# Kernel tuning notes

Hardware: AMD Instinct MI355X
Metric: run time of the kernel (lower is better)

## Reference

```python
import jax, jax.numpy as jnp
import numpy as np
import math

D_MODEL = 1024
N_HEADS = 16
D_HEAD = D_MODEL // N_HEADS


def setup_inputs() -> dict:
    key = jax.random.key(0)
    ks = jax.random.split(key, 5)
    B, T, C = 4, 2048, D_MODEL
    s = 1.0 / math.sqrt(C)
    return {
        "x": jax.random.normal(ks[0], (B, T, C), dtype=jnp.float32),
        "qkv_w": jax.random.normal(ks[1], (3 * C, C), dtype=jnp.float32) * s,
        "qkv_b": jnp.zeros((3 * C,), dtype=jnp.float32),
        "out_w": jax.random.normal(ks[2], (C, C), dtype=jnp.float32) * s,
        "out_b": jnp.zeros((C,), dtype=jnp.float32),
    }


def reference(x, qkv_w, qkv_b, out_w, out_b):
    B, T, C = x.shape
    H, Dh = N_HEADS, D_HEAD
    qkv = x @ qkv_w.T + qkv_b              # [B,T,3C] (torch Linear: x W^T + b)
    q, k, v = jnp.split(qkv, 3, axis=-1)
    # [B,T,C] -> [B,H,T,Dh]
    q = q.reshape(B, T, H, Dh).transpose(0, 2, 1, 3)
    k = k.reshape(B, T, H, Dh).transpose(0, 2, 1, 3)
    v = v.reshape(B, T, H, Dh).transpose(0, 2, 1, 3)
    att = jnp.einsum("bhqd,bhkd->bhqk", q, k) / math.sqrt(Dh)
    causal = jnp.tril(jnp.ones((T, T), dtype=bool))  # True = keep
    att = jnp.where(causal, att, -jnp.inf)
    att = jax.nn.softmax(att, axis=-1)
    y = jnp.einsum("bhqk,bhkd->bhqd", att, v)
    y = y.transpose(0, 2, 1, 3).reshape(B, T, C)
    return y @ out_w.T + out_b
```

## Files before the change

### kernel.cpp

```cpp
#include <hip/hip_runtime.h>

typedef __attribute__((ext_vector_type(4))) float f32x4;
typedef __attribute__((ext_vector_type(16))) float f32x16;
typedef __attribute__((ext_vector_type(8))) __bf16 bf16x8;
typedef __attribute__((ext_vector_type(4))) __bf16 bf16x4;
typedef __attribute__((ext_vector_type(2))) unsigned u32x2;

#define MFMA_B16(a,b,c) __builtin_amdgcn_mfma_f32_16x16x32_bf16((a),(b),(c),0,0,0)
#define MFMA32(a,b,c)  __builtin_amdgcn_mfma_f32_32x32x16_bf16((a),(b),(c),0,0,0)

static constexpr int T_LEN  = 2048;
static constexpr int C_DIM  = 1024;
static constexpr int H_NUM  = 16;
static constexpr int D_HEADc = 64;
static constexpr float Q_PRESCALE = 0.125f * 1.4426950408889634f;

__device__ __forceinline__ void async16(const void* g, void* l) {
  __builtin_amdgcn_global_load_lds(
      (const __attribute__((address_space(1))) unsigned int*)g,
      (__attribute__((address_space(3))) unsigned int*)l, 16, 0, 0);
}

__device__ __forceinline__ unsigned cvtpk(float lo, float hi) {
  unsigned r;
  asm("v_cvt_pk_bf16_f32 %0, %1, %2" : "=v"(r) : "v"(lo), "v"(hi));
  return r;
}

__global__ __launch_bounds__(256) void cvt_kernel(const float* __restrict__ s,
                                                  __bf16* __restrict__ d, int n4) {
  int i = blockIdx.x * 256 + threadIdx.x;
  if (i >= n4) return;
  float4 f = reinterpret_cast<const float4*>(s)[i];
  bf16x4 o;
  o.x = (__bf16)f.x; o.y = (__bf16)f.y; o.z = (__bf16)f.z; o.w = (__bf16)f.w;
  reinterpret_cast<bf16x4*>(d)[i] = o;
}

__global__ __launch_bounds__(256) void gemm_qkv(const __bf16* __restrict__ A,
                                                const __bf16* __restrict__ W,
                                                const float* __restrict__ bias,
                                                __bf16* __restrict__ qb,
                                                __bf16* __restrict__ kb,
                                                __bf16* __restrict__ vb) {
  constexpr int K = 1024;
  __shared__ __bf16 As[128 * 64];
  __shared__ __bf16 Bs[128 * 64];
  const int tid = threadIdx.x;
  const int wid = tid >> 6, lane = tid & 63, l16 = lane & 15, lg = lane >> 4;
  const int r8 = lane >> 3, sl = lane & 7;
  const int r7 = l16 & 7;
  const int wm = wid >> 1, wn = wid & 1;
  const int m0 = blockIdx.x * 128, n0 = blockIdx.y * 128;

  f32x4 acc[4][4];
#pragma unroll
  for (int i = 0; i < 4; ++i)
#pragma unroll
    for (int j = 0; j < 4; ++j) acc[i][j] = f32x4{0.f, 0.f, 0.f, 0.f};

  for (int k0 = 0; k0 < K; k0 += 64) {
    __builtin_amdgcn_s_barrier();
#pragma unroll
    for (int it = 0; it < 4; ++it) {
      int chunk = it * 4 + wid;
      int row = chunk * 8 + r8;
      int scol = ((sl ^ (row & 7)) << 3);
      async16(A + (long)(m0 + row) * K + k0 + scol, &As[chunk * 512]);
      async16(W + (long)(n0 + row) * K + k0 + scol, &Bs[chunk * 512]);
    }
    asm volatile("s_waitcnt vmcnt(0)" ::: "memory");
    __builtin_amdgcn_s_barrier();
#pragma unroll
    for (int kt = 0; kt < 2; ++kt) {
      const int sw = ((((kt << 2) | lg) ^ r7) << 3);
      bf16x8 af[4], bfv[4];
#pragma unroll
      for (int mi = 0; mi < 4; ++mi)
        af[mi] = *reinterpret_cast<const bf16x8*>(&As[(wm * 64 + mi * 16 + l16) * 64 + sw]);
#pragma unroll
      for (int nt = 0; nt < 4; ++nt)
        bfv[nt] = *reinterpret_cast<const bf16x8*>(&Bs[(wn * 64 + nt * 16 + l16) * 64 + sw]);
#pragma unroll
      for (int mi = 0; mi < 4; ++mi)
#pragma unroll
        for (int nt = 0; nt < 4; ++nt)
          acc[mi][nt] = MFMA_B16(af[mi], bfv[nt], acc[mi][nt]);
    }
  }
#pragma unroll
  for (int mi = 0; mi < 4; ++mi)
#pragma unroll
    for (int nt = 0; nt < 4; ++nt)
#pragma unroll
      for (int r = 0; r < 4; ++r) {
        int m = m0 + wm * 64 + mi * 16 + lg * 4 + r;
        int n = n0 + wn * 64 + nt * 16 + l16;
        float val = acc[mi][nt][r] + bias[n];
        int which = n >> 10;
        int cc = n & 1023;
        int h = cc >> 6, d = cc & 63;
        long b = m >> 11;
        long t = m & 2047;
        if (which == 0) {
          qb[(((b * H_NUM + h) * T_LEN) + t) * D_HEADc + d] = (__bf16)(val * Q_PRESCALE);
        } else if (which == 1) {
          kb[(((b * H_NUM + h) * T_LEN) + t) * D_HEADc + d] = (__bf16)val;
        } else {
          vb[(((b * H_NUM + h) * D_HEADc) + d) * T_LEN + t] = (__bf16)val;
        }
      }
}

__global__ __launch_bounds__(256) void attn_kernel(const __bf16* __restrict__ q,
                                                   const __bf16* __restrict__ k,
                                                   const __bf16* __restrict__ vt,
                                                   __bf16* __restrict__ y) {
  __shared__ __bf16 Ks[2][64 * 64];
  __shared__ __bf16 Vs[2][64 * 64];
  const int tid = threadIdx.x;
  const int wid = tid >> 6, lane = tid & 63;
  const int l31 = lane & 31, hi = lane >> 5;
  const int r8 = lane >> 3, sl = lane & 7;
  const int r7 = l31 & 7;
  const int bid = blockIdx.x;
  const int qt = 15 - (bid >> 6);
  const int bh = bid & 63;
  const int q0 = qt * 128;
  const int qw = q0 + wid * 32;
  const int qglob = qw + l31;
  const __bf16* qg = q + (long)bh * T_LEN * D_HEADc;
  const __bf16* kg = k + (long)bh * T_LEN * D_HEADc;
  const __bf16* vg = vt + (long)bh * T_LEN * D_HEADc;

  bf16x8 qf[4];
#pragma unroll
  for (int dt = 0; dt < 4; ++dt)
    qf[dt] = *reinterpret_cast<const bf16x8*>(
        qg + (long)qglob * D_HEADc + dt * 16 + hi * 8);

  f32x16 o[2];
#pragma unroll
  for (int di = 0; di < 2; ++di)
#pragma unroll
    for (int r = 0; r < 16; ++r) o[di][r] = 0.f;
  float m = -3e38f, l = 0.f;

  auto stage = [&](int buf, int t) {
    const int k0s = t * 64;
#pragma unroll
    for (int it = 0; it < 2; ++it) {
      int chunk = it * 4 + wid;
      int row = chunk * 8 + r8;
      int scol = ((sl ^ (row & 7)) << 3);
      async16(kg + (long)(k0s + row) * D_HEADc + scol, &Ks[buf][chunk * 512]);
      async16(vg + (long)row * T_LEN + k0s + scol, &Vs[buf][chunk * 512]);
    }
  };

  const int ntiles = qt * 2 + 2;
  stage(0, 0);
  int cur = 0;
  for (int t = 0; t < ntiles; ++t) {
    if (t + 1 < ntiles) {
      stage(cur ^ 1, t + 1);
      asm volatile("s_waitcnt vmcnt(4)" ::: "memory");
    } else {
      asm volatile("s_waitcnt vmcnt(0)" ::: "memory");
    }
    __builtin_amdgcn_s_barrier();
    const int k0 = t * 64;
    if (k0 < qw + 32) {
      f32x16 s[2];
#pragma unroll
      for (int ki = 0; ki < 2; ++ki)
#pragma unroll
        for (int r = 0; r < 16; ++r) s[ki][r] = 0.f;
      __builtin_amdgcn_s_setprio(1);
#pragma unroll
      for (int dt = 0; dt < 4; ++dt) {
        const int swz = (((dt << 1) | hi) ^ r7) << 3;
        bf16x8 kf0 = *reinterpret_cast<const bf16x8*>(&Ks[cur][l31 * 64 + swz]);
        bf16x8 kf1 = *reinterpret_cast<const bf16x8*>(&Ks[cur][(32 + l31) * 64 + swz]);
        s[0] = MFMA32(kf0, qf[dt], s[0]);
        s[1] = MFMA32(kf1, qf[dt], s[1]);
      }
      __builtin_amdgcn_s_setprio(0);

      if (k0 + 63 > qw) {
#pragma unroll
        for (int r = 0; r < 16; ++r) {
          const int kb = (r & 3) + 8 * (r >> 2) + 4 * hi;
          if (k0 + kb > qglob) s[0][r] = -3e38f;
          if (k0 + 32 + kb > qglob) s[1][r] = -3e38f;
        }
      }
      float mx = -3e38f;
#pragma unroll
      for (int r = 0; r < 16; ++r) mx = fmaxf(mx, fmaxf(s[0][r], s[1][r]));
      mx = fmaxf(mx, __shfl_xor(mx, 32));
      if (!__all(mx <= m + 8.f)) {
        const float mn = fmaxf(m, mx);
        const float al = exp2f(m - mn);
        m = mn;
        l *= al;
#pragma unroll
        for (int di = 0; di < 2; ++di)
#pragma unroll
          for (int r = 0; r < 16; ++r) o[di][r] *= al;
      }
      float ls = 0.f;
      unsigned pb[4][4];
#pragma unroll
      for (int ki = 0; ki < 2; ++ki) {
#pragma unroll
        for (int r = 0; r < 16; ++r) {
          float e = exp2f(s[ki][r] - m);
          ls += e;
          s[ki][r] = e;
        }
        unsigned d0 = cvtpk(s[ki][0], s[ki][1]),   d1 = cvtpk(s[ki][2], s[ki][3]);
        unsigned d2 = cvtpk(s[ki][4], s[ki][5]),   d3 = cvtpk(s[ki][6], s[ki][7]);
        unsigned d4 = cvtpk(s[ki][8], s[ki][9]),   d5 = cvtpk(s[ki][10], s[ki][11]);
        unsigned d6 = cvtpk(s[ki][12], s[ki][13]), d7 = cvtpk(s[ki][14], s[ki][15]);
        u32x2 a = __builtin_amdgcn_permlane32_swap(d0, d2, false, false);
        u32x2 b = __builtin_amdgcn_permlane32_swap(d1, d3, false, false);
        pb[ki * 2][0] = a[0]; pb[ki * 2][1] = b[0];
        pb[ki * 2][2] = a[1]; pb[ki * 2][3] = b[1];
        u32x2 c = __builtin_amdgcn_permlane32_swap(d4, d6, false, false);
        u32x2 d = __builtin_amdgcn_permlane32_swap(d5, d7, false, false);
        pb[ki * 2 + 1][0] = c[0]; pb[ki * 2 + 1][1] = d[0];
        pb[ki * 2 + 1][2] = c[1]; pb[ki * 2 + 1][3] = d[1];
      }
      ls += __shfl_xor(ls, 32);
      l += ls;

      __builtin_amdgcn_s_setprio(1);
#pragma unroll
      for (int kt = 0; kt < 4; ++kt) {
        union { unsigned u[4]; bf16x8 v; } pu;
        pu.u[0] = pb[kt][0]; pu.u[1] = pb[kt][1];
        pu.u[2] = pb[kt][2]; pu.u[3] = pb[kt][3];
        const int swz = (((kt << 1) | hi) ^ r7) << 3;
        bf16x8 vf0 = *reinterpret_cast<const bf16x8*>(&Vs[cur][l31 * 64 + swz]);
        bf16x8 vf1 = *reinterpret_cast<const bf16x8*>(&Vs[cur][(32 + l31) * 64 + swz]);
        o[0] = MFMA32(vf0, pu.v, o[0]);
        o[1] = MFMA32(vf1, pu.v, o[1]);
      }
      __builtin_amdgcn_s_setprio(0);
    }
    __builtin_amdgcn_s_barrier();
    cur ^= 1;
  }

  const long bb = bh >> 4;
  const int h = bh & 15;
  const float inv = 1.f / l;
  const long row = bb * T_LEN + qglob;
#pragma unroll
  for (int di = 0; di < 2; ++di)
#pragma unroll
    for (int rr = 0; rr < 4; ++rr) {
      bf16x4 pk;
#pragma unroll
      for (int c = 0; c < 4; ++c) pk[c] = (__bf16)(o[di][rr * 4 + c] * inv);
      *reinterpret_cast<bf16x4*>(
          &y[row * C_DIM + h * D_HEADc + di * 32 + rr * 8 + hi * 4]) = pk;
    }
}

__global__ __launch_bounds__(256) void gemm_proj(const __bf16* __restrict__ A,
                                                 const __bf16* __restrict__ W,
                                                 const float* __restrict__ bias,
                                                 float* __restrict__ out) {
  constexpr int K = 1024;
  __shared__ __bf16 As[128 * 64];
  __shared__ __bf16 Bs[128 * 64];
  const int tid = threadIdx.x;
  const int wid = tid >> 6, lane = tid & 63, l16 = lane & 15, lg = lane >> 4;
  const int r8 = lane >> 3, sl = lane & 7;
  const int r7 = l16 & 7;
  const int wm = wid >> 1, wn = wid & 1;
  const int m0 = blockIdx.x * 128, n0 = blockIdx.y * 128;

  f32x4 acc[4][4];
#pragma unroll
  for (int i = 0; i < 4; ++i)
#pragma unroll
    for (int j = 0; j < 4; ++j) acc[i][j] = f32x4{0.f, 0.f, 0.f, 0.f};

  for (int k0 = 0; k0 < K; k0 += 64) {
    __builtin_amdgcn_s_barrier();
#pragma unroll
    for (int it = 0; it < 4; ++it) {
      int chunk = it * 4 + wid;
      int row = chunk * 8 + r8;
      int scol = ((sl ^ (row & 7)) << 3);
      async16(A + (long)(m0 + row) * K + k0 + scol, &As[chunk * 512]);
      async16(W + (long)(n0 + row) * K + k0 + scol, &Bs[chunk * 512]);
    }
    asm volatile("s_waitcnt vmcnt(0)" ::: "memory");
    __builtin_amdgcn_s_barrier();
#pragma unroll
    for (int kt = 0; kt < 2; ++kt) {
      const int sw = ((((kt << 2) | lg) ^ r7) << 3);
      bf16x8 af[4], bfv[4];
#pragma unroll
      for (int mi = 0; mi < 4; ++mi)
        af[mi] = *reinterpret_cast<const bf16x8*>(&As[(wm * 64 + mi * 16 + l16) * 64 + sw]);
#pragma unroll
      for (int nt = 0; nt < 4; ++nt)
        bfv[nt] = *reinterpret_cast<const bf16x8*>(&Bs[(wn * 64 + nt * 16 + l16) * 64 + sw]);
#pragma unroll
      for (int mi = 0; mi < 4; ++mi)
#pragma unroll
        for (int nt = 0; nt < 4; ++nt)
          acc[mi][nt] = MFMA_B16(af[mi], bfv[nt], acc[mi][nt]);
    }
  }
#pragma unroll
  for (int mi = 0; mi < 4; ++mi)
#pragma unroll
    for (int nt = 0; nt < 4; ++nt)
#pragma unroll
      for (int r = 0; r < 4; ++r) {
        long m = m0 + wm * 64 + mi * 16 + lg * 4 + r;
        int n = n0 + wn * 64 + nt * 16 + l16;
        out[m * C_DIM + n] = acc[mi][nt][r] + bias[n];
      }
}

extern "C" void kernel_launch(void* const* d_in, const int* in_sizes, int n_in,
                              void* d_out, int out_size, void* d_ws, size_t ws_size,
                              hipStream_t stream) {
  const float* x     = (const float*)d_in[0];
  const float* qkv_w = (const float*)d_in[1];
  const float* qkv_b = (const float*)d_in[2];
  const float* out_w = (const float*)d_in[3];
  const float* out_b = (const float*)d_in[4];
  float* out = (float*)d_out;

  const long NX  = 8192L * 1024;
  const long NWQ = 3072L * 1024;
  const long NWO = 1024L * 1024;
  const size_t need = (size_t)(5 * NX + NWQ + NWO) * 2;
  if (ws_size < need) return;

  __bf16* xb   = (__bf16*)d_ws;
  __bf16* wqkv = xb + NX;
  __bf16* wout = wqkv + NWQ;
  __bf16* qb   = wout + NWO;
  __bf16* kb   = qb + NX;
  __bf16* vb   = kb + NX;
  __bf16* yb   = vb + NX;

  cvt_kernel<<<(int)(NX / 4 / 256), 256, 0, stream>>>(x, xb, (int)(NX / 4));
  cvt_kernel<<<(int)(NWQ / 4 / 256), 256, 0, stream>>>(qkv_w, wqkv, (int)(NWQ / 4));
  cvt_kernel<<<(int)(NWO / 4 / 256), 256, 0, stream>>>(out_w, wout, (int)(NWO / 4));

  gemm_qkv<<<dim3(64, 24), 256, 0, stream>>>(xb, wqkv, qkv_b, qb, kb, vb);
  attn_kernel<<<dim3(1024), 256, 0, stream>>>(qb, kb, vb, yb);
  gemm_proj<<<dim3(64, 8), 256, 0, stream>>>(yb, wout, out_b, out);
}
```

Baseline: 196.4 us.

## Pair causal query tiles per block, fuse casts, and compute row sums via MFMA

The attention kernel now launches half as many blocks, and each block handles two query tiles (qt and 15-qt) in sequence so every block does the same causal work. The row-sum of softmax probabilities moves from scalar adds plus a shuffle to an extra MFMA against a vector of ones, and the row-max becomes a tree reduction. The three float-to-bf16 conversion launches become one kernel. In exchange there are fewer resident blocks, so latency hiding may drop, and each tile pair runs serially with a pipeline restart between phases.

```diff
diff --git a/kernel.cpp b/kernel.cpp
--- a/kernel.cpp
+++ b/kernel.cpp
@@ -27,14 +27,21 @@
   return r;
 }
 
-__global__ __launch_bounds__(256) void cvt_kernel(const float* __restrict__ s,
-                                                  __bf16* __restrict__ d, int n4) {
+__global__ __launch_bounds__(256) void cvt3_kernel(const float* __restrict__ a, __bf16* __restrict__ da, int na,
+                                                   const float* __restrict__ b, __bf16* __restrict__ db, int nb,
+                                                   const float* __restrict__ c, __bf16* __restrict__ dc, int nc) {
   int i = blockIdx.x * 256 + threadIdx.x;
-  if (i >= n4) return;
-  float4 f = reinterpret_cast<const float4*>(s)[i];
+  const float* s;
+  __bf16* d;
+  long j;
+  if (i < na) { s = a; d = da; j = i; }
+  else if (i < na + nb) { s = b; d = db; j = i - na; }
+  else if (i < na + nb + nc) { s = c; d = dc; j = i - na - nb; }
+  else return;
+  float4 f = reinterpret_cast<const float4*>(s)[j];
   bf16x4 o;
   o.x = (__bf16)f.x; o.y = (__bf16)f.y; o.z = (__bf16)f.z; o.w = (__bf16)f.w;
-  reinterpret_cast<bf16x4*>(d)[i] = o;
+  reinterpret_cast<bf16x4*>(d)[j] = o;
 }
 
 __global__ __launch_bounds__(256) void gemm_qkv(const __bf16* __restrict__ A,
@@ -124,27 +131,22 @@
   const int r8 = lane >> 3, sl = lane & 7;
   const int r7 = l31 & 7;
   const int bid = blockIdx.x;
-  const int qt = 15 - (bid >> 6);
+  const int pair = bid >> 6;
   const int bh = bid & 63;
-  const int q0 = qt * 128;
-  const int qw = q0 + wid * 32;
-  const int qglob = qw + l31;
   const __bf16* qg = q + (long)bh * T_LEN * D_HEADc;
   const __bf16* kg = k + (long)bh * T_LEN * D_HEADc;
   const __bf16* vg = vt + (long)bh * T_LEN * D_HEADc;
-
-  bf16x8 qf[4];
-#pragma unroll
-  for (int dt = 0; dt < 4; ++dt)
-    qf[dt] = *reinterpret_cast<const bf16x8*>(
-        qg + (long)qglob * D_HEADc + dt * 16 + hi * 8);
-
-  f32x16 o[2];
-#pragma unroll
-  for (int di = 0; di < 2; ++di)
-#pragma unroll
-    for (int r = 0; r < 16; ++r) o[di][r] = 0.f;
-  float m = -3e38f, l = 0.f;
+  const long bb = bh >> 4;
+  const int h = bh & 15;
+
+  union { unsigned short us[8]; bf16x8 v; } ones_u;
+#pragma unroll
+  for (int i = 0; i < 8; ++i) ones_u.us[i] = 0x3F80;
+  const bf16x8 ones = ones_u.v;
+
+  f32x16 z16;
+#pragma unroll
+  for (int r = 0; r < 16; ++r) z16[r] = 0.f;
 
   auto stage = [&](int buf, int t) {
     const int k0s = t * 64;
@@ -158,115 +160,141 @@
     }
   };
 
-  const int ntiles = qt * 2 + 2;
-  stage(0, 0);
-  int cur = 0;
-  for (int t = 0; t < ntiles; ++t) {
-    if (t + 1 < ntiles) {
-      stage(cur ^ 1, t + 1);
-      asm volatile("s_waitcnt vmcnt(4)" ::: "memory");
-    } else {
-      asm volatile("s_waitcnt vmcnt(0)" ::: "memory");
-    }
-    __builtin_amdgcn_s_barrier();
-    const int k0 = t * 64;
-    if (k0 < qw + 32) {
-      f32x16 s[2];
-#pragma unroll
-      for (int ki = 0; ki < 2; ++ki)
-#pragma unroll
-        for (int r = 0; r < 16; ++r) s[ki][r] = 0.f;
-      __builtin_amdgcn_s_setprio(1);
-#pragma unroll
-      for (int dt = 0; dt < 4; ++dt) {
-        const int swz = (((dt << 1) | hi) ^ r7) << 3;
-        bf16x8 kf0 = *reinterpret_cast<const bf16x8*>(&Ks[cur][l31 * 64 + swz]);
-        bf16x8 kf1 = *reinterpret_cast<const bf16x8*>(&Ks[cur][(32 + l31) * 64 + swz]);
-        s[0] = MFMA32(kf0, qf[dt], s[0]);
-        s[1] = MFMA32(kf1, qf[dt], s[1]);
-      }
-      __builtin_amdgcn_s_setprio(0);
-
-      if (k0 + 63 > qw) {
-#pragma unroll
-        for (int r = 0; r < 16; ++r) {
-          const int kb = (r & 3) + 8 * (r >> 2) + 4 * hi;
-          if (k0 + kb > qglob) s[0][r] = -3e38f;
-          if (k0 + 32 + kb > qglob) s[1][r] = -3e38f;
-        }
-      }
-      float mx = -3e38f;
-#pragma unroll
-      for (int r = 0; r < 16; ++r) mx = fmaxf(mx, fmaxf(s[0][r], s[1][r]));
-      mx = fmaxf(mx, __shfl_xor(mx, 32));
-      if (!__all(mx <= m + 8.f)) {
-        const float mn = fmaxf(m, mx);
-        const float al = exp2f(m - mn);
-        m = mn;
-        l *= al;
-#pragma unroll
-        for (int di = 0; di < 2; ++di)
-#pragma unroll
-          for (int r = 0; r < 16; ++r) o[di][r] *= al;
-      }
-      float ls = 0.f;
-      unsigned pb[4][4];
-#pragma unroll
-      for (int ki = 0; ki < 2; ++ki) {
-#pragma unroll
-        for (int r = 0; r < 16; ++r) {
-          float e = exp2f(s[ki][r] - m);
-          ls += e;
-          s[ki][r] = e;
-        }
-        unsigned d0 = cvtpk(s[ki][0], s[ki][1]),   d1 = cvtpk(s[ki][2], s[ki][3]);
-        unsigned d2 = cvtpk(s[ki][4], s[ki][5]),   d3 = cvtpk(s[ki][6], s[ki][7]);
-        unsigned d4 = cvtpk(s[ki][8], s[ki][9]),   d5 = cvtpk(s[ki][10], s[ki][11]);
-        unsigned d6 = cvtpk(s[ki][12], s[ki][13]), d7 = cvtpk(s[ki][14], s[ki][15]);
-        u32x2 a = __builtin_amdgcn_permlane32_swap(d0, d2, false, false);
-        u32x2 b = __builtin_amdgcn_permlane32_swap(d1, d3, false, false);
-        pb[ki * 2][0] = a[0]; pb[ki * 2][1] = b[0];
-        pb[ki * 2][2] = a[1]; pb[ki * 2][3] = b[1];
-        u32x2 c = __builtin_amdgcn_permlane32_swap(d4, d6, false, false);
-        u32x2 d = __builtin_amdgcn_permlane32_swap(d5, d7, false, false);
-        pb[ki * 2 + 1][0] = c[0]; pb[ki * 2 + 1][1] = d[0];
-        pb[ki * 2 + 1][2] = c[1]; pb[ki * 2 + 1][3] = d[1];
-      }
-      ls += __shfl_xor(ls, 32);
-      l += ls;
-
-      __builtin_amdgcn_s_setprio(1);
-#pragma unroll
-      for (int kt = 0; kt < 4; ++kt) {
-        union { unsigned u[4]; bf16x8 v; } pu;
-        pu.u[0] = pb[kt][0]; pu.u[1] = pb[kt][1];
-        pu.u[2] = pb[kt][2]; pu.u[3] = pb[kt][3];
-        const int swz = (((kt << 1) | hi) ^ r7) << 3;
-        bf16x8 vf0 = *reinterpret_cast<const bf16x8*>(&Vs[cur][l31 * 64 + swz]);
-        bf16x8 vf1 = *reinterpret_cast<const bf16x8*>(&Vs[cur][(32 + l31) * 64 + swz]);
-        o[0] = MFMA32(vf0, pu.v, o[0]);
-        o[1] = MFMA32(vf1, pu.v, o[1]);
-      }
-      __builtin_amdgcn_s_setprio(0);
-    }
-    __builtin_amdgcn_s_barrier();
-    cur ^= 1;
+  auto m3 = [](float a, float b, float c) { return fmaxf(fmaxf(a, b), c); };
+
+  for (int ph = 0; ph < 2; ++ph) {
+    const int qt = ph ? (15 - pair) : pair;
+    const int q0 = qt * 128;
+    const int qw = q0 + wid * 32;
+    const int qglob = qw + l31;
+
+    bf16x8 qf[4];
+#pragma unroll
+    for (int dt = 0; dt < 4; ++dt)
+      qf[dt] = *reinterpret_cast<const bf16x8*>(qg + (long)qglob * D_HEADc + dt * 16 + hi * 8);
+
+    f32x16 o[2];
+    o[0] = z16; o[1] = z16;
+    f32x16 lacc = z16;
+    float m = -3e38f;
+
+    const int ntiles = qt * 2 + 2;
+    stage(0, 0);
+    int cur = 0;
+    for (int t = 0; t < ntiles; ++t) {
+      if (t + 1 < ntiles) {
+        stage(cur ^ 1, t + 1);
+        asm volatile("s_waitcnt vmcnt(4)" ::: "memory");
+      } else {
+        asm volatile("s_waitcnt vmcnt(0)" ::: "memory");
+      }
+      __builtin_amdgcn_s_barrier();
+      const int k0 = t * 64;
+      if (k0 < qw + 32) {
+        f32x16 s[2];
+        __builtin_amdgcn_s_setprio(1);
+        {
+          const int swz = (hi ^ r7) << 3;
+          bf16x8 kf0 = *reinterpret_cast<const bf16x8*>(&Ks[cur][l31 * 64 + swz]);
+          bf16x8 kf1 = *reinterpret_cast<const bf16x8*>(&Ks[cur][(32 + l31) * 64 + swz]);
+          s[0] = MFMA32(kf0, qf[0], z16);
+          s[1] = MFMA32(kf1, qf[0], z16);
+        }
+#pragma unroll
+        for (int dt = 1; dt < 4; ++dt) {
+          const int swz = (((dt << 1) | hi) ^ r7) << 3;
+          bf16x8 kf0 = *reinterpret_cast<const bf16x8*>(&Ks[cur][l31 * 64 + swz]);
+          bf16x8 kf1 = *reinterpret_cast<const bf16x8*>(&Ks[cur][(32 + l31) * 64 + swz]);
+          s[0] = MFMA32(kf0, qf[dt], s[0]);
+          s[1] = MFMA32(kf1, qf[dt], s[1]);
+        }
+        __builtin_amdgcn_s_setprio(0);
+
+        if (k0 + 63 > qw) {
+#pragma unroll
+          for (int r = 0; r < 16; ++r) {
+            const int kb = (r & 3) + 8 * (r >> 2) + 4 * hi;
+            if (k0 + kb > qglob) s[0][r] = -3e38f;
+            if (k0 + 32 + kb > qglob) s[1][r] = -3e38f;
+          }
+        }
+
+        float xv[11];
+#pragma unroll
+        for (int g = 0; g < 5; ++g) xv[g] = m3(s[0][3 * g], s[0][3 * g + 1], s[0][3 * g + 2]);
+        xv[5] = m3(s[0][15], s[1][0], s[1][1]);
+#pragma unroll
+        for (int g = 0; g < 4; ++g) xv[6 + g] = m3(s[1][2 + 3 * g], s[1][3 + 3 * g], s[1][4 + 3 * g]);
+        xv[10] = fmaxf(s[1][14], s[1][15]);
+        float w0 = m3(xv[0], xv[1], xv[2]), w1 = m3(xv[3], xv[4], xv[5]);
+        float w2 = m3(xv[6], xv[7], xv[8]), w3 = fmaxf(xv[9], xv[10]);
+        float mx = fmaxf(m3(w0, w1, w2), w3);
+        mx = fmaxf(mx, __shfl_xor(mx, 32));
+
+        if (!__all(mx <= m + 8.f)) {
+          const float mn = fmaxf(m, mx);
+          const float al = exp2f(m - mn);
+          m = mn;
+          lacc[0] *= al;
+#pragma unroll
+          for (int di = 0; di < 2; ++di)
+#pragma unroll
+            for (int r = 0; r < 16; ++r) o[di][r] *= al;
+        }
+#pragma unroll
+        for (int ki = 0; ki < 2; ++ki)
+#pragma unroll
+          for (int r = 0; r < 16; ++r) s[ki][r] = exp2f(s[ki][r] - m);
+
+        unsigned pb[4][4];
+#pragma unroll
+        for (int ki = 0; ki < 2; ++ki) {
+          unsigned d0 = cvtpk(s[ki][0], s[ki][1]),   d1 = cvtpk(s[ki][2], s[ki][3]);
+          unsigned d2 = cvtpk(s[ki][4], s[ki][5]),   d3 = cvtpk(s[ki][6], s[ki][7]);
+          unsigned d4 = cvtpk(s[ki][8], s[ki][9]),   d5 = cvtpk(s[ki][10], s[ki][11]);
+          unsigned d6 = cvtpk(s[ki][12], s[ki][13]), d7 = cvtpk(s[ki][14], s[ki][15]);
+          u32x2 a2 = __builtin_amdgcn_permlane32_swap(d0, d2, false, false);
+          u32x2 b2 = __builtin_amdgcn_permlane32_swap(d1, d3, false, false);
+          pb[ki * 2][0] = a2[0]; pb[ki * 2][1] = b2[0];
+          pb[ki * 2][2] = a2[1]; pb[ki * 2][3] = b2[1];
+          u32x2 c2 = __builtin_amdgcn_permlane32_swap(d4, d6, false, false);
+          u32x2 e2 = __builtin_amdgcn_permlane32_swap(d5, d7, false, false);
+          pb[ki * 2 + 1][0] = c2[0]; pb[ki * 2 + 1][1] = e2[0];
+          pb[ki * 2 + 1][2] = c2[1]; pb[ki * 2 + 1][3] = e2[1];
+        }
+
+        __builtin_amdgcn_s_setprio(1);
+#pragma unroll
+        for (int kt = 0; kt < 4; ++kt) {
+          union { unsigned u[4]; bf16x8 v; } pu;
+#pragma unroll
+          for (int w = 0; w < 4; ++w) pu.u[w] = pb[kt][w];
+          const int swz = (((kt << 1) | hi) ^ r7) << 3;
+          bf16x8 vf0 = *reinterpret_cast<const bf16x8*>(&Vs[cur][l31 * 64 + swz]);
+          bf16x8 vf1 = *reinterpret_cast<const bf16x8*>(&Vs[cur][(32 + l31) * 64 + swz]);
+          o[0] = MFMA32(vf0, pu.v, o[0]);
+          o[1] = MFMA32(vf1, pu.v, o[1]);
+          lacc = MFMA32(ones, pu.v, lacc);
+        }
+        __builtin_amdgcn_s_setprio(0);
+      }
+      __builtin_amdgcn_s_barrier();
+      cur ^= 1;
+    }
+
+    const float inv = 1.f / lacc[0];
+    const long row = bb * T_LEN + qglob;
+#pragma unroll
+    for (int di = 0; di < 2; ++di)
+#pragma unroll
+      for (int rr = 0; rr < 4; ++rr) {
+        bf16x4 pk;
+#pragma unroll
+        for (int c = 0; c < 4; ++c) pk[c] = (__bf16)(o[di][rr * 4 + c] * inv);
+        *reinterpret_cast<bf16x4*>(
+            &y[row * C_DIM + h * D_HEADc + di * 32 + rr * 8 + hi * 4]) = pk;
+      }
   }
-
-  const long bb = bh >> 4;
-  const int h = bh & 15;
-  const float inv = 1.f / l;
-  const long row = bb * T_LEN + qglob;
-#pragma unroll
-  for (int di = 0; di < 2; ++di)
-#pragma unroll
-    for (int rr = 0; rr < 4; ++rr) {
-      bf16x4 pk;
-#pragma unroll
-      for (int c = 0; c < 4; ++c) pk[c] = (__bf16)(o[di][rr * 4 + c] * inv);
-      *reinterpret_cast<bf16x4*>(
-          &y[row * C_DIM + h * D_HEADc + di * 32 + rr * 8 + hi * 4]) = pk;
-    }
 }
 
 __global__ __launch_bounds__(256) void gemm_proj(const __bf16* __restrict__ A,
@@ -354,11 +382,10 @@
   __bf16* vb   = kb + NX;
   __bf16* yb   = vb + NX;
 
-  cvt_kernel<<<(int)(NX / 4 / 256), 256, 0, stream>>>(x, xb, (int)(NX / 4));
-  cvt_kernel<<<(int)(NWQ / 4 / 256), 256, 0, stream>>>(qkv_w, wqkv, (int)(NWQ / 4));
-  cvt_kernel<<<(int)(NWO / 4 / 256), 256, 0, stream>>>(out_w, wout, (int)(NWO / 4));
+  const int na = (int)(NX / 4), nb = (int)(NWQ / 4), nc = (int)(NWO / 4);
+  cvt3_kernel<<<(na + nb + nc + 255) / 256, 256, 0, stream>>>(x, xb, na, qkv_w, wqkv, nb, out_w, wout, nc);
 
   gemm_qkv<<<dim3(64, 24), 256, 0, stream>>>(xb, wqkv, qkv_b, qb, kb, vb);
-  attn_kernel<<<dim3(1024), 256, 0, stream>>>(qb, kb, vb, yb);
+  attn_kernel<<<dim3(512), 256, 0, stream>>>(qb, kb, vb, yb);
   gemm_proj<<<dim3(64, 8), 256, 0, stream>>>(yb, wout, out_b, out);
 }
```

After: 199.3 us. No clear change (+1.5%).
